# Kernel optimization log

Hardware: AMD Instinct MI355X
Metric: run time of the kernel (lower is better)

Reference implementation:

```python
import jax, jax.numpy as jnp
import numpy as np

# Static config matching init_kwargs / input_specs
IN_CH = 256
PATCH = 64
LAYERS = 4
B, H, W = 4, 256, 256
IC = IN_CH // 4        # SelfAttention inner channels (reduce=4)
C16 = IN_CH // 16      # f_test conv output channels
ALPHA = 0.05


def conv1x1(x, w, b):
    # x: (b,c,h,w), w: (out,c), b: (out,)  == nn.Conv2d(c,out,1)
    return jnp.einsum('bchw,oc->bohw', x, w) + b[None, :, None, None]


def setup_inputs() -> dict:
    key = jax.random.key(0)
    ks = jax.random.split(key, 12)
    s = 0.05
    return {
        'x':  jax.random.normal(ks[0], (B, IN_CH, H, W), jnp.float32),
        'Wq': jax.random.normal(ks[1], (IC, IN_CH), jnp.float32) * s,
        'bq': jax.random.normal(ks[2], (IC,), jnp.float32) * s,
        'Wk': jax.random.normal(ks[3], (IC, IN_CH), jnp.float32) * s,
        'bk': jax.random.normal(ks[4], (IC,), jnp.float32) * s,
        'Wv': jax.random.normal(ks[5], (IC, IN_CH), jnp.float32) * s,
        'bv': jax.random.normal(ks[6], (IC,), jnp.float32) * s,
        'Wr': jax.random.normal(ks[7], (IN_CH, IC), jnp.float32) * s,
        'br': jax.random.normal(ks[8], (IN_CH,), jnp.float32) * s,
        'Wf': jax.random.normal(ks[9], (C16, IN_CH), jnp.float32) * s,
        'bf': jax.random.normal(ks[10], (C16,), jnp.float32) * s,
    }


def reference(x, Wq, bq, Wk, bk, Wv, bv, Wr, br, Wf, bf):
    b, c, h, w = x.shape
    p = PATCH
    nh = h // p
    ic = IC

    # f_test applies the same 1x1 conv to the FULL image every call; its output
    # is identical each time, so precompute the per-(batch,channel) mean/var once.
    # torch uses .detach() -> stop_gradient.
    y2 = jax.lax.stop_gradient(conv1x1(x, Wf, bf))           # (b, C16, h, w)
    m2 = y2.mean(axis=(2, 3))                                 # (b, C16)
    v2 = y2.var(axis=(2, 3))                                  # biased var
    n1 = float(p * p)
    n2 = float(h * w)
    dfw = n1 + n2 - 2.0

    def ftest_decision(patch):
        # Two-group one-way ANOVA (scipy.stats.f_oneway) per (batch, channel).
        y1 = jax.lax.stop_gradient(conv1x1(patch, Wf, bf))    # (b, C16, p, p)
        m1 = y1.mean(axis=(2, 3))
        v1 = y1.var(axis=(2, 3))
        gm = (n1 * m1 + n2 * m2) / (n1 + n2)
        ssb = n1 * (m1 - gm) ** 2 + n2 * (m2 - gm) ** 2       # df_between = 1
        ssw = n1 * v1 + n2 * v2                               # sum sq dev within
        Fst = ssb / (ssw / dfw)
        # p-value = sf of F(1, dfw) = I_{dfw/(dfw+F)}(dfw/2, 1/2)
        pval = jax.scipy.special.betainc(dfw / 2.0, 0.5, dfw / (dfw + Fst))
        counts = jnp.sum(pval < ALPHA)
        return counts * 2 >= m1.size                          # scalar bool

    def attn(patch):
        # SelfAttention.forward: channel-to-channel attention over a patch.
        Q = conv1x1(patch, Wq, bq).reshape(b, ic, p * p)      # (b, ic, pp)
        # NOTE: original does K_pro.view(b, -1, inner_ch) -- a raw reshape,
        # NOT a transpose; we reproduce that exactly.
        K = conv1x1(patch, Wk, bk).reshape(b, p * p, ic)      # (b, pp, ic)
        V = conv1x1(patch, Wv, bv).reshape(b, ic, p * p)
        wts = jax.nn.softmax(jnp.einsum('bim,bmj->bij', Q, K), axis=1)  # (b,ic,ic)
        att = jnp.einsum('bij,bjm->bim', wts, V).reshape(b, ic, p, p)
        return conv1x1(att, Wr, br) + patch

    def run_patch(patch):
        # layer loop with data-dependent early break, expressed via masking
        stopped = jnp.array(False)
        for _ in range(LAYERS):
            stopped = stopped | ftest_decision(patch)  # break BEFORE attention
            patch = jnp.where(stopped, patch, attn(patch))
        return patch

    # Extract all nh*nh patches: (n_patches, b, c, p, p)
    patches = (x.reshape(b, c, nh, p, nh, p)
                .transpose(2, 4, 0, 1, 3, 5)
                .reshape(nh * nh, b, c, p, p))
    out_patches = jax.vmap(run_patch)(patches)

    # Faithful to original bug: x1 = x.clone() happens inside the patch loop,
    # so only the LAST patch's update survives in the returned tensor.
    x1 = x.at[:, :, (nh - 1) * p:, (nh - 1) * p:].set(out_patches[-1])
    return x1
```

## Files before the change

### kernel.cpp

```cpp
#include <hip/hip_runtime.h>

#define FCRIT 3.8415923532

#define OFF_FULL   0u
#define OFF_PATCH  1024u
#define OFF_S      8192u
#define OFF_Y3     1048576u
#define STATS_ZERO_BYTES 270336u

static __device__ __forceinline__ double wred(double v) {
#pragma unroll
  for (int off = 32; off > 0; off >>= 1) v += __shfl_down(v, off, 64);
  return v;
}

static __device__ __forceinline__ bool is_stopped(const double* __restrict__ fullS,
                                                  const double* __restrict__ patchS,
                                                  int upto) {
  const int k = threadIdx.x & 63;
  const double fs = fullS[2 * k], fq = fullS[2 * k + 1];
  const double m2 = fs * (1.0 / 65536.0);
  const double v2 = fq * (1.0 / 65536.0) - m2 * m2;
  bool stopped = false;
  for (int l = 0; l <= upto; ++l) {
    const double* ps = patchS + (size_t)l * 128;
    const double s1 = ps[2 * k], s2 = ps[2 * k + 1];
    const double m1 = s1 * (1.0 / 4096.0);
    const double v1 = s2 * (1.0 / 4096.0) - m1 * m1;
    const double gm = (4096.0 * m1 + 65536.0 * m2) * (1.0 / 69632.0);
    const double d1 = m1 - gm, d2 = m2 - gm;
    const double ssb = 4096.0 * d1 * d1 + 65536.0 * d2 * d2;
    const double ssw = 4096.0 * v1 + 65536.0 * v2;
    const double F = ssb * (69630.0 / ssw);
    const unsigned long long bal = __ballot(F > FCRIT);
    const int cnt = __popcll(bal);
    stopped = stopped || (2 * cnt >= 64);
  }
  return stopped;
}

static __device__ __forceinline__ void fma16(float acc[4][4], float4 w, float4 v) {
  const float wa[4] = {w.x, w.y, w.z, w.w};
  const float va[4] = {v.x, v.y, v.z, v.w};
#pragma unroll
  for (int a = 0; a < 4; ++a)
#pragma unroll
    for (int c = 0; c < 4; ++c) acc[a][c] += wa[a] * va[c];
}

static __device__ __forceinline__ size_t pidx(int b, int c, int y, int x) {
  return (((size_t)b * 256 + c) * 256 + 192 + y) * 256 + 192 + x;
}

__global__ __launch_bounds__(256) void k_main(const float* __restrict__ x,
                                              const float* __restrict__ Wf,
                                              const float* __restrict__ bf,
                                              float* __restrict__ out,
                                              double* __restrict__ fullS,
                                              double* __restrict__ patchS0) {
  __shared__ __align__(16) float WfT2[16 * 257];
  __shared__ __align__(16) float WfT[256 * 16];
  __shared__ double sm[4][16][2];
  __shared__ double sp[4][16][2];
  const int t = threadIdx.x;
  const int bb = blockIdx.x >> 7;
  const int rp = blockIdx.x & 127;

  for (int r = 0; r < 16; ++r) {
    int idx = r * 256 + t;
    WfT2[(idx >> 8) * 257 + (idx & 255)] = Wf[idx];
  }
  __syncthreads();
  for (int r = 0; r < 16; ++r) {
    int idx = r * 256 + t;
    int c = idx >> 4, o = idx & 15;
    WfT[c * 16 + o] = WfT2[o * 257 + c];
  }
  __syncthreads();

  const int r0 = rp * 2 + (t >> 7);
  const int col2 = (t & 127) * 2;
  const size_t base = (size_t)bb * 16777216 + (size_t)r0 * 256 + col2;
  const float* xp = x + base;
  float* op = out + base;
  const bool pStore = (rp >= 96) && ((t & 127) >= 96);

  float y0[16], y1[16];
#pragma unroll
  for (int o = 0; o < 16; ++o) { y0[o] = 0.f; y1[o] = 0.f; }

  for (int cb = 0; cb < 32; ++cb) {
    double v[8];
#pragma unroll
    for (int u = 0; u < 8; ++u)
      v[u] = *reinterpret_cast<const double*>(xp + (size_t)(cb * 8 + u) * 65536);
#pragma unroll
    for (int u = 0; u < 8; ++u) {
      double* dst = reinterpret_cast<double*>(op + (size_t)(cb * 8 + u) * 65536);
      if (pStore) *dst = v[u];
      else __builtin_nontemporal_store(v[u], dst);
      const int c = cb * 8 + u;
      float2 f = *reinterpret_cast<const float2*>(&v[u]);
      const float4* wf = reinterpret_cast<const float4*>(&WfT[c * 16]);
      const float4 w0 = wf[0], w1 = wf[1], w2 = wf[2], w3 = wf[3];
      const float wv[16] = {w0.x, w0.y, w0.z, w0.w, w1.x, w1.y, w1.z, w1.w,
                            w2.x, w2.y, w2.z, w2.w, w3.x, w3.y, w3.z, w3.w};
#pragma unroll
      for (int o = 0; o < 16; ++o) {
        y0[o] += wv[o] * f.x;
        y1[o] += wv[o] * f.y;
      }
    }
  }

  const int w = t >> 6, lane = t & 63;
  const bool pBlock = (rp >= 96);
  const bool pLane = ((t & 127) >= 96);
#pragma unroll 1
  for (int o = 0; o < 16; ++o) {
    const float bo = bf[o];
    const double a0 = (double)(y0[o] + bo), a1 = (double)(y1[o] + bo);
    double s1 = a0 + a1, s2 = a0 * a0 + a1 * a1;
    const double r1 = wred(s1), r2 = wred(s2);
    if (lane == 0) { sm[w][o][0] = r1; sm[w][o][1] = r2; }
    if (pBlock) {
      double p1 = pLane ? s1 : 0.0, p2 = pLane ? s2 : 0.0;
      p1 = wred(p1); p2 = wred(p2);
      if (lane == 0) { sp[w][o][0] = p1; sp[w][o][1] = p2; }
    }
  }
  __syncthreads();
  if (t < 32) {
    const int o = t >> 1, wh = t & 1;
    double s = sm[0][o][wh] + sm[1][o][wh] + sm[2][o][wh] + sm[3][o][wh];
    unsafeAtomicAdd(&fullS[(bb * 16 + o) * 2 + wh], s);
    if (pBlock) {
      double p = sp[0][o][wh] + sp[1][o][wh] + sp[2][o][wh] + sp[3][o][wh];
      unsafeAtomicAdd(&patchS0[(bb * 16 + o) * 2 + wh], p);
    }
  }
}

__global__ __launch_bounds__(256) void k_qkv(const float* __restrict__ out,
                                             const float* __restrict__ Wq, const float* __restrict__ bq,
                                             const float* __restrict__ Wk, const float* __restrict__ bk,
                                             const float* __restrict__ Wv, const float* __restrict__ bv,
                                             float* __restrict__ Y3,
                                             const double* __restrict__ fullS,
                                             const double* __restrict__ patchS, int layer) {
  if (is_stopped(fullS, patchS, layer)) return;
  __shared__ __align__(16) float W3T[64][68];
  __shared__ __align__(16) float X2[64 * 64];
  const int t = threadIdx.x;
  const int blk = blockIdx.x;
  const int qt = blk & 63;
  const int mt = (blk >> 6) % 3;
  const int bb = blk / 192;
  const float* Wm = (mt == 0) ? Wq : (mt == 1) ? Wk : Wv;
  const float* bm = (mt == 0) ? bq : (mt == 1) ? bk : bv;
  const int tq = t & 15, to = t >> 4;
  float acc[4][4] = {};
  for (int kc = 0; kc < 4; ++kc) {
    const int k0 = kc * 64;
    __syncthreads();
    for (int r = 0; r < 16; ++r) {
      int idx = r * 256 + t;
      int ml = idx >> 6, kl = idx & 63;
      W3T[kl][ml] = Wm[ml * 256 + k0 + kl];
    }
    for (int r = 0; r < 16; ++r) {
      int idx = r * 256 + t;
      int kl = idx >> 6, ql = idx & 63;
      X2[kl * 64 + ql] = out[pidx(bb, k0 + kl, qt, ql)];
    }
    __syncthreads();
#pragma unroll 8
    for (int kk = 0; kk < 64; ++kk) {
      const float4 wv = *reinterpret_cast<const float4*>(&W3T[kk][to * 4]);
      const float4 xv = *reinterpret_cast<const float4*>(&X2[kk * 64 + tq * 4]);
      fma16(acc, wv, xv);
    }
  }
#pragma unroll
  for (int a = 0; a < 4; ++a) {
    const int ml = to * 4 + a;
    const float bias = bm[ml];
    float4 res;
    res.x = acc[a][0] + bias;
    res.y = acc[a][1] + bias;
    res.z = acc[a][2] + bias;
    res.w = acc[a][3] + bias;
    *reinterpret_cast<float4*>(&Y3[((size_t)bb * 192 + mt * 64 + ml) * 4096 + qt * 64 + tq * 4]) = res;
  }
}

__global__ __launch_bounds__(256) void k_s(const float* __restrict__ Y3,
                                           float* __restrict__ Sbase,
                                           const double* __restrict__ fullS,
                                           const double* __restrict__ patchS, int layer) {
  if (is_stopped(fullS, patchS, layer)) return;
  __shared__ __align__(16) float QT[64][68];
  __shared__ __align__(16) float K2[64 * 64];
  const int t = threadIdx.x;
  const int mc = blockIdx.x & 63;
  const int bb = blockIdx.x >> 6;
  const int m0 = mc * 64;
  const float* Q = Y3 + (size_t)bb * 192 * 4096;
  const float* Kf = Q + 64 * 4096;
  for (int r = 0; r < 16; ++r) {
    int idx = r * 256 + t;
    int i = idx >> 6, ml = idx & 63;
    QT[ml][i] = Q[(size_t)i * 4096 + m0 + ml];
  }
  for (int r = 0; r < 16; ++r) {
    int idx = r * 256 + t;
    K2[idx] = Kf[(size_t)m0 * 64 + idx];
  }
  __syncthreads();
  const int tj = t & 15, ti = t >> 4;
  float acc[4][4] = {};
#pragma unroll 8
  for (int mm = 0; mm < 64; ++mm) {
    const float4 qv = *reinterpret_cast<const float4*>(&QT[mm][ti * 4]);
    const float4 kv = *reinterpret_cast<const float4*>(&K2[mm * 64 + tj * 4]);
    fma16(acc, qv, kv);
  }
  float* Sl = Sbase + (size_t)layer * 16384 + bb * 4096;
#pragma unroll
  for (int a = 0; a < 4; ++a)
#pragma unroll
    for (int c = 0; c < 4; ++c)
      unsafeAtomicAdd(&Sl[(ti * 4 + a) * 64 + tj * 4 + c], acc[a][c]);
}

__global__ __launch_bounds__(256) void k_awr(const float* __restrict__ Y3,
                                             const float* __restrict__ Sbase,
                                             const float* __restrict__ Wr,
                                             const float* __restrict__ br,
                                             float* __restrict__ out,
                                             const double* __restrict__ fullS,
                                             const double* __restrict__ patchS, int layer) {
  if (is_stopped(fullS, patchS, layer)) return;
  __shared__ __align__(16) float Sw[64 * 68];
  __shared__ __align__(16) float AV[64 * 68];
  __shared__ __align__(16) float WrF[128 * 65];
  const int t = threadIdx.x;
  const int y = blockIdx.x & 63;
  const int oh = (blockIdx.x >> 6) & 1;
  const int bb = blockIdx.x >> 7;

  const float* Vp = Y3 + (size_t)bb * 192 * 4096 + (size_t)128 * 4096 + y * 64;
  for (int r = 0; r < 16; ++r) {
    int idx = r * 256 + t;
    int j = idx >> 6, xx = idx & 63;
    AV[j * 68 + xx] = Vp[(size_t)j * 4096 + xx];
  }
  const float* Sl = Sbase + (size_t)layer * 16384 + bb * 4096;
  for (int r = 0; r < 16; ++r) {
    int idx = r * 256 + t;
    Sw[(idx & 63) * 68 + (idx >> 6)] = Sl[idx];
  }
  for (int r = 0; r < 32; ++r) {
    int idx = r * 256 + t;
    int ol = idx >> 6, i = idx & 63;
    WrF[ol * 65 + i] = Wr[(oh * 128 + ol) * 64 + i];
  }
  __syncthreads();

  if (t < 64) {
    float* colp = &Sw[t * 68];
    float mx = -1e30f;
#pragma unroll
    for (int i = 0; i < 64; ++i) mx = fmaxf(mx, colp[i]);
    float sum = 0.f;
#pragma unroll
    for (int i = 0; i < 64; ++i) {
      float e = __expf(colp[i] - mx);
      colp[i] = e;
      sum += e;
    }
    const float inv = 1.f / sum;
#pragma unroll
    for (int i = 0; i < 64; ++i) colp[i] *= inv;
  }
  __syncthreads();

  {
    const int ti = t >> 4, tx = t & 15;
    float acc[4][4] = {};
#pragma unroll 8
    for (int j = 0; j < 64; ++j) {
      const float4 wv = *reinterpret_cast<const float4*>(&Sw[j * 68 + ti * 4]);
      const float4 vv = *reinterpret_cast<const float4*>(&AV[j * 68 + tx * 4]);
      fma16(acc, wv, vv);
    }
    __syncthreads();
#pragma unroll
    for (int a = 0; a < 4; ++a) {
      float4 res;
      res.x = acc[a][0]; res.y = acc[a][1]; res.z = acc[a][2]; res.w = acc[a][3];
      *reinterpret_cast<float4*>(&AV[(ti * 4 + a) * 68 + tx * 4]) = res;
    }
  }
  __syncthreads();

  const int to = t >> 3, tx8 = t & 7;
  float acc[4][8] = {};
#pragma unroll 4
  for (int i = 0; i < 64; ++i) {
    const float4 a0 = *reinterpret_cast<const float4*>(&AV[i * 68 + tx8 * 8]);
    const float4 a1 = *reinterpret_cast<const float4*>(&AV[i * 68 + tx8 * 8 + 4]);
    const float av[8] = {a0.x, a0.y, a0.z, a0.w, a1.x, a1.y, a1.z, a1.w};
#pragma unroll
    for (int a = 0; a < 4; ++a) {
      const float wv = WrF[(to * 4 + a) * 65 + i];
#pragma unroll
      for (int c = 0; c < 8; ++c) acc[a][c] += wv * av[c];
    }
  }
#pragma unroll
  for (int a = 0; a < 4; ++a) {
    const int o = oh * 128 + to * 4 + a;
    const float bro = br[o];
    float* p = out + pidx(bb, o, y, tx8 * 8);
    float4 p0 = *reinterpret_cast<const float4*>(p);
    float4 p1 = *reinterpret_cast<const float4*>(p + 4);
    p0.x += acc[a][0] + bro; p0.y += acc[a][1] + bro;
    p0.z += acc[a][2] + bro; p0.w += acc[a][3] + bro;
    p1.x += acc[a][4] + bro; p1.y += acc[a][5] + bro;
    p1.z += acc[a][6] + bro; p1.w += acc[a][7] + bro;
    *reinterpret_cast<float4*>(p) = p0;
    *reinterpret_cast<float4*>(p + 4) = p1;
  }
}

__global__ __launch_bounds__(256) void k_ftest(const float* __restrict__ out,
                                               const float* __restrict__ Wf,
                                               const float* __restrict__ bf,
                                               double* __restrict__ patchS,
                                               const double* __restrict__ fullS, int layer) {
  if (is_stopped(fullS, patchS, layer)) return;
  __shared__ __align__(16) float WfT2[16 * 257];
  __shared__ __align__(16) float WfT[256 * 16];
  __shared__ float part[2 * 128 * 17];
  __shared__ double red[16][16][2];
  const int t = threadIdx.x;
  const int bb = blockIdx.x >> 5;
  const int rg = blockIdx.x & 31;

  for (int r = 0; r < 16; ++r) {
    int idx = r * 256 + t;
    WfT2[(idx >> 8) * 257 + (idx & 255)] = Wf[idx];
  }
  __syncthreads();
  for (int r = 0; r < 16; ++r) {
    int idx = r * 256 + t;
    int c = idx >> 4, o = idx & 15;
    WfT[c * 16 + o] = WfT2[o * 257 + c];
  }
  __syncthreads();

  const int h = t >> 7;
  const int px = t & 127;
  const int row = 192 + rg * 2 + (px >> 6);
  const int col = 192 + (px & 63);
  const size_t base = (size_t)bb * 16777216 + (size_t)h * 128 * 65536 + (size_t)row * 256 + col;

  float y[16] = {};
  for (int cb = 0; cb < 16; ++cb) {
    float v[8];
#pragma unroll
    for (int u = 0; u < 8; ++u)
      v[u] = out[base + (size_t)(cb * 8 + u) * 65536];
#pragma unroll
    for (int u = 0; u < 8; ++u) {
      const int c = h * 128 + cb * 8 + u;
      const float4* wf = reinterpret_cast<const float4*>(&WfT[c * 16]);
      const float4 w0 = wf[0], w1 = wf[1], w2 = wf[2], w3 = wf[3];
      const float wv[16] = {w0.x, w0.y, w0.z, w0.w, w1.x, w1.y, w1.z, w1.w,
                            w2.x, w2.y, w2.z, w2.w, w3.x, w3.y, w3.z, w3.w};
#pragma unroll
      for (int o = 0; o < 16; ++o) y[o] += wv[o] * v[u];
    }
  }
#pragma unroll
  for (int o = 0; o < 16; ++o) part[(h * 128 + px) * 17 + o] = y[o];
  __syncthreads();

  const int oo = t & 15, pxg = t >> 4;
  double s1 = 0.0, s2 = 0.0;
  const float bo = bf[oo];
#pragma unroll
  for (int j = 0; j < 8; ++j) {
    const int p = pxg * 8 + j;
    const float yv = part[p * 17 + oo] + part[(128 + p) * 17 + oo] + bo;
    const double v = (double)yv;
    s1 += v;
    s2 += v * v;
  }
  red[oo][pxg][0] = s1;
  red[oo][pxg][1] = s2;
  __syncthreads();
  if (t < 32) {
    const int o = t >> 1, wh = t & 1;
    double s = 0.0;
#pragma unroll
    for (int g = 0; g < 16; ++g) s += red[o][g][wh];
    unsafeAtomicAdd(&patchS[(size_t)(layer + 1) * 128 + (bb * 16 + o) * 2 + wh], s);
  }
}

extern "C" void kernel_launch(void* const* d_in, const int* in_sizes, int n_in,
                              void* d_out, int out_size, void* d_ws, size_t ws_size,
                              hipStream_t stream) {
  const float* x  = (const float*)d_in[0];
  const float* Wq = (const float*)d_in[1];
  const float* bq = (const float*)d_in[2];
  const float* Wk = (const float*)d_in[3];
  const float* bk = (const float*)d_in[4];
  const float* Wv = (const float*)d_in[5];
  const float* bv = (const float*)d_in[6];
  const float* Wr = (const float*)d_in[7];
  const float* br = (const float*)d_in[8];
  const float* Wf = (const float*)d_in[9];
  const float* bf = (const float*)d_in[10];
  float* out = (float*)d_out;
  char* ws = (char*)d_ws;

  double* fullS  = (double*)(ws + OFF_FULL);
  double* patchS = (double*)(ws + OFF_PATCH);
  float* Sb = (float*)(ws + OFF_S);
  float* Y3 = (float*)(ws + OFF_Y3);

  (void)hipMemsetAsync(ws, 0, STATS_ZERO_BYTES, stream);
  k_main<<<512, 256, 0, stream>>>(x, Wf, bf, out, fullS, patchS);
  for (int l = 0; l < 4; ++l) {
    k_qkv<<<768, 256, 0, stream>>>(out, Wq, bq, Wk, bk, Wv, bv, Y3, fullS, patchS, l);
    k_s<<<256, 256, 0, stream>>>(Y3, Sb, fullS, patchS, l);
    k_awr<<<512, 256, 0, stream>>>(Y3, Sb, Wr, br, out, fullS, patchS, l);
    if (l < 3) k_ftest<<<128, 256, 0, stream>>>(out, Wf, bf, patchS, fullS, l);
  }
}
```

Baseline: 260.7 us.

## Use split-bf16 MFMA for QKV projection with pre-converted operands

The fp32 SIMT QKV projection is replaced by bf16 MFMA using a three-level bf16 split (hi/mid/lo) of both weights and activations, with six cross products to approximate fp32 accuracy. A new kernel transposes and converts the patch activations into pixel-major bf16 triples each layer, and the weights are converted once per call. This trades tensor-core throughput against an extra kernel launch, about 3x the activation bytes written and read, and slightly reduced accuracy.

```diff
diff --git a/kernel.cpp b/kernel.cpp
--- a/kernel.cpp
+++ b/kernel.cpp
@@ -6,12 +6,28 @@
 #define OFF_PATCH  1024u
 #define OFF_S      8192u
 #define OFF_Y3     1048576u
+#define OFF_XH     16777216u
+#define OFF_WH     41943040u
 #define STATS_ZERO_BYTES 270336u
+
+typedef __attribute__((ext_vector_type(8))) short short8;
+typedef __attribute__((ext_vector_type(8))) unsigned short us8;
+typedef __attribute__((ext_vector_type(4))) float f32x4;
 
 static __device__ __forceinline__ double wred(double v) {
 #pragma unroll
   for (int off = 32; off > 0; off >>= 1) v += __shfl_down(v, off, 64);
   return v;
+}
+
+static __device__ __forceinline__ unsigned short f2bf(float f) {
+  union { float f; unsigned u; } v; v.f = f;
+  unsigned r = v.u + 0x7fffu + ((v.u >> 16) & 1u);
+  return (unsigned short)(r >> 16);
+}
+static __device__ __forceinline__ float bf2f(unsigned short h) {
+  union { unsigned u; float f; } v; v.u = ((unsigned)h) << 16;
+  return v.f;
 }
 
 static __device__ __forceinline__ bool is_stopped(const double* __restrict__ fullS,
@@ -52,6 +68,29 @@
   return (((size_t)b * 256 + c) * 256 + 192 + y) * 256 + 192 + x;
 }
 
+__global__ __launch_bounds__(256) void k_wcvt(const float* __restrict__ Wq,
+                                              const float* __restrict__ Wk,
+                                              const float* __restrict__ Wv,
+                                              unsigned short* __restrict__ Whml) {
+  const int idx0 = (blockIdx.x * 256 + threadIdx.x) * 4;
+#pragma unroll
+  for (int u = 0; u < 4; ++u) {
+    const int i = idx0 + u;
+    const int row = i >> 8, col = i & 255;
+    const float v = (row < 64) ? Wq[row * 256 + col]
+                  : (row < 128) ? Wk[(row - 64) * 256 + col]
+                                : Wv[(row - 128) * 256 + col];
+    const unsigned short h = f2bf(v);
+    const float r1 = v - bf2f(h);
+    const unsigned short m = f2bf(r1);
+    const float r2 = r1 - bf2f(m);
+    const unsigned short l = f2bf(r2);
+    Whml[i] = h;
+    Whml[49152 + i] = m;
+    Whml[98304 + i] = l;
+  }
+}
+
 __global__ __launch_bounds__(256) void k_main(const float* __restrict__ x,
                                               const float* __restrict__ Wf,
                                               const float* __restrict__ bf,
@@ -141,57 +180,122 @@
   }
 }
 
-__global__ __launch_bounds__(256) void k_qkv(const float* __restrict__ out,
-                                             const float* __restrict__ Wq, const float* __restrict__ bq,
-                                             const float* __restrict__ Wk, const float* __restrict__ bk,
-                                             const float* __restrict__ Wv, const float* __restrict__ bv,
+__global__ __launch_bounds__(256) void k_xcvt(const float* __restrict__ out,
+                                              unsigned short* __restrict__ Xhml,
+                                              const double* __restrict__ fullS,
+                                              const double* __restrict__ patchS, int layer) {
+  if (is_stopped(fullS, patchS, layer)) return;
+  __shared__ float T[256 * 65];
+  const int t = threadIdx.x;
+  const int bb = blockIdx.x >> 6;
+  const int y = blockIdx.x & 63;
+  for (int r = 0; r < 64; ++r) {
+    int idx = r * 256 + t;
+    T[(idx >> 6) * 65 + (idx & 63)] = out[pidx(bb, idx >> 6, y, idx & 63)];
+  }
+  __syncthreads();
+  const int px = t >> 2, c0 = (t & 3) * 64;
+  const size_t dstbase = ((size_t)bb * 4096 + y * 64 + px) * 256 + c0;
+#pragma unroll 1
+  for (int g = 0; g < 8; ++g) {
+    us8 hv, mv, lv;
+#pragma unroll
+    for (int j = 0; j < 8; ++j) {
+      const float v = T[(c0 + g * 8 + j) * 65 + px];
+      const unsigned short h = f2bf(v);
+      const float r1 = v - bf2f(h);
+      const unsigned short m = f2bf(r1);
+      const float r2 = r1 - bf2f(m);
+      const unsigned short l = f2bf(r2);
+      hv[j] = (unsigned short)h; mv[j] = m; lv[j] = l;
+    }
+    *reinterpret_cast<us8*>(Xhml + dstbase + g * 8) = hv;
+    *reinterpret_cast<us8*>(Xhml + 4194304u + dstbase + g * 8) = mv;
+    *reinterpret_cast<us8*>(Xhml + 8388608u + dstbase + g * 8) = lv;
+  }
+}
+
+__global__ __launch_bounds__(256) void k_qkv(const unsigned short* __restrict__ Whml,
+                                             const float* __restrict__ bq,
+                                             const float* __restrict__ bk,
+                                             const float* __restrict__ bv,
+                                             const unsigned short* __restrict__ Xhml,
                                              float* __restrict__ Y3,
                                              const double* __restrict__ fullS,
                                              const double* __restrict__ patchS, int layer) {
   if (is_stopped(fullS, patchS, layer)) return;
-  __shared__ __align__(16) float W3T[64][68];
-  __shared__ __align__(16) float X2[64 * 64];
+  __shared__ __align__(16) unsigned short Al[3][64][40];
+  __shared__ __align__(16) unsigned short Bl[3][128][40];
   const int t = threadIdx.x;
-  const int blk = blockIdx.x;
-  const int qt = blk & 63;
-  const int mt = (blk >> 6) % 3;
-  const int bb = blk / 192;
-  const float* Wm = (mt == 0) ? Wq : (mt == 1) ? Wk : Wv;
-  const float* bm = (mt == 0) ? bq : (mt == 1) ? bk : bv;
-  const int tq = t & 15, to = t >> 4;
-  float acc[4][4] = {};
-  for (int kc = 0; kc < 4; ++kc) {
-    const int k0 = kc * 64;
+  const int nt = blockIdx.x & 31;
+  const int mt = (blockIdx.x >> 5) % 3;
+  const int bb = blockIdx.x / 96;
+  const int w = t >> 6, lane = t & 63;
+  const int lo16 = lane & 15, hi4 = lane >> 4;
+
+  f32x4 acc[4][2];
+#pragma unroll
+  for (int mf = 0; mf < 4; ++mf)
+#pragma unroll
+    for (int nf = 0; nf < 2; ++nf) acc[mf][nf] = (f32x4)0.f;
+
+  const unsigned short* Wbase = Whml + mt * 64 * 256;
+  const unsigned short* Xbase = Xhml + ((size_t)bb * 4096 + nt * 128) * 256;
+  const int am = t >> 2, ak = (t & 3) * 8;
+  const int bpx = t >> 1, bkh = (t & 1) * 16;
+
+  for (int kc = 0; kc < 8; ++kc) {
+    const int k0 = kc * 32;
     __syncthreads();
-    for (int r = 0; r < 16; ++r) {
-      int idx = r * 256 + t;
-      int ml = idx >> 6, kl = idx & 63;
-      W3T[kl][ml] = Wm[ml * 256 + k0 + kl];
-    }
-    for (int r = 0; r < 16; ++r) {
-      int idx = r * 256 + t;
-      int kl = idx >> 6, ql = idx & 63;
-      X2[kl * 64 + ql] = out[pidx(bb, k0 + kl, qt, ql)];
+#pragma unroll
+    for (int lev = 0; lev < 3; ++lev) {
+      const us8 va = *reinterpret_cast<const us8*>(Wbase + lev * 49152 + am * 256 + k0 + ak);
+      *reinterpret_cast<us8*>(&Al[lev][am][ak]) = va;
+      const unsigned short* s = Xbase + (size_t)lev * 4194304 + (size_t)bpx * 256 + k0 + bkh;
+      const us8 v0 = *reinterpret_cast<const us8*>(s);
+      const us8 v1 = *reinterpret_cast<const us8*>(s + 8);
+      *reinterpret_cast<us8*>(&Bl[lev][bpx][bkh]) = v0;
+      *reinterpret_cast<us8*>(&Bl[lev][bpx][bkh + 8]) = v1;
     }
     __syncthreads();
-#pragma unroll 8
-    for (int kk = 0; kk < 64; ++kk) {
-      const float4 wv = *reinterpret_cast<const float4*>(&W3T[kk][to * 4]);
-      const float4 xv = *reinterpret_cast<const float4*>(&X2[kk * 64 + tq * 4]);
-      fma16(acc, wv, xv);
-    }
-  }
-#pragma unroll
-  for (int a = 0; a < 4; ++a) {
-    const int ml = to * 4 + a;
-    const float bias = bm[ml];
-    float4 res;
-    res.x = acc[a][0] + bias;
-    res.y = acc[a][1] + bias;
-    res.z = acc[a][2] + bias;
-    res.w = acc[a][3] + bias;
-    *reinterpret_cast<float4*>(&Y3[((size_t)bb * 192 + mt * 64 + ml) * 4096 + qt * 64 + tq * 4]) = res;
-  }
+
+    short8 af[3][4], bfr[3][2];
+    const int koff = hi4 * 8;
+#pragma unroll
+    for (int lev = 0; lev < 3; ++lev) {
+#pragma unroll
+      for (int mf = 0; mf < 4; ++mf)
+        af[lev][mf] = *reinterpret_cast<const short8*>(&Al[lev][mf * 16 + lo16][koff]);
+#pragma unroll
+      for (int nf = 0; nf < 2; ++nf)
+        bfr[lev][nf] = *reinterpret_cast<const short8*>(&Bl[lev][w * 32 + nf * 16 + lo16][koff]);
+    }
+#pragma unroll
+    for (int mf = 0; mf < 4; ++mf)
+#pragma unroll
+      for (int nf = 0; nf < 2; ++nf) {
+        f32x4 c = acc[mf][nf];
+        c = __builtin_amdgcn_mfma_f32_16x16x32_bf16(af[0][mf], bfr[0][nf], c, 0, 0, 0);
+        c = __builtin_amdgcn_mfma_f32_16x16x32_bf16(af[0][mf], bfr[1][nf], c, 0, 0, 0);
+        c = __builtin_amdgcn_mfma_f32_16x16x32_bf16(af[1][mf], bfr[0][nf], c, 0, 0, 0);
+        c = __builtin_amdgcn_mfma_f32_16x16x32_bf16(af[0][mf], bfr[2][nf], c, 0, 0, 0);
+        c = __builtin_amdgcn_mfma_f32_16x16x32_bf16(af[2][mf], bfr[0][nf], c, 0, 0, 0);
+        c = __builtin_amdgcn_mfma_f32_16x16x32_bf16(af[1][mf], bfr[1][nf], c, 0, 0, 0);
+        acc[mf][nf] = c;
+      }
+  }
+
+  const float* bias = (mt == 0) ? bq : (mt == 1) ? bk : bv;
+#pragma unroll
+  for (int mf = 0; mf < 4; ++mf)
+#pragma unroll
+    for (int nf = 0; nf < 2; ++nf)
+#pragma unroll
+      for (int r = 0; r < 4; ++r) {
+        const int mrow = mf * 16 + hi4 * 4 + r;
+        const int col = nt * 128 + w * 32 + nf * 16 + lo16;
+        Y3[((size_t)bb * 192 + mt * 64 + mrow) * 4096 + col] = acc[mf][nf][r] + bias[mrow];
+      }
 }
 
 __global__ __launch_bounds__(256) void k_s(const float* __restrict__ Y3,
@@ -431,11 +535,15 @@
   double* patchS = (double*)(ws + OFF_PATCH);
   float* Sb = (float*)(ws + OFF_S);
   float* Y3 = (float*)(ws + OFF_Y3);
+  unsigned short* Xhml = (unsigned short*)(ws + OFF_XH);
+  unsigned short* Whml = (unsigned short*)(ws + OFF_WH);
 
   (void)hipMemsetAsync(ws, 0, STATS_ZERO_BYTES, stream);
+  k_wcvt<<<48, 256, 0, stream>>>(Wq, Wk, Wv, Whml);
   k_main<<<512, 256, 0, stream>>>(x, Wf, bf, out, fullS, patchS);
   for (int l = 0; l < 4; ++l) {
-    k_qkv<<<768, 256, 0, stream>>>(out, Wq, bq, Wk, bk, Wv, bv, Y3, fullS, patchS, l);
+    k_xcvt<<<256, 256, 0, stream>>>(out, Xhml, fullS, patchS, l);
+    k_qkv<<<384, 256, 0, stream>>>(Whml, bq, bk, bv, Xhml, Y3, fullS, patchS, l);
     k_s<<<256, 256, 0, stream>>>(Y3, Sb, fullS, patchS, l);
     k_awr<<<512, 256, 0, stream>>>(Y3, Sb, Wr, br, out, fullS, patchS, l);
     if (l < 3) k_ftest<<<128, 256, 0, stream>>>(out, Wf, bf, patchS, fullS, l);
```

After: 252.4 us. 1.03x faster.
